# Kernel optimization log

Hardware: AMD Instinct MI355X
Metric: run time of the kernel (lower is better)

## Reference

```python
import jax, jax.numpy as jnp
import numpy as np

W_WIN = 21  # window size (init arg w)
N_HEADS = 8
HEAD_DIM = 64

def setup_inputs() -> dict:
    key = jax.random.key(0)
    ks = jax.random.split(key, 6)
    b, c, l, d = 8, 2, 2048, 512
    x = jax.random.normal(ks[0], (b, c, l, d), dtype=jnp.float32)
    Wqkv = jax.random.normal(ks[1], (d, 3 * d), dtype=jnp.float32) * (1.0 / np.sqrt(d))
    bqkv = jax.random.normal(ks[2], (3 * d,), dtype=jnp.float32) * 0.02
    bias_rw = jax.random.uniform(ks[3], (N_HEADS, HEAD_DIM), dtype=jnp.float32,
                                 minval=-1.0 / np.sqrt(HEAD_DIM), maxval=1.0 / np.sqrt(HEAD_DIM))
    Wout = jax.random.normal(ks[4], (d, d), dtype=jnp.float32) * (1.0 / np.sqrt(d))
    bout = jax.random.normal(ks[5], (d,), dtype=jnp.float32) * 0.02
    return {"x": x, "Wqkv": Wqkv, "bqkv": bqkv, "bias_rw": bias_rw, "Wout": Wout, "bout": bout}

def reference(x, Wqkv, bqkv, bias_rw, Wout, bout):
    b, c, l, d = x.shape
    H, hd = bias_rw.shape
    B = b * c
    w_half = W_WIN // 2

    xf = x.reshape(B, l, d)
    qkv = xf @ Wqkv + bqkv                      # [B, l, 3d]
    q, k, v = jnp.split(qkv, 3, axis=-1)
    q = q.reshape(B, l, H, hd) * (hd ** -0.5)
    k = k.reshape(B, l, H, hd)
    v = v.reshape(B, l, H, hd)

    qk = q + bias_rw                            # bias_r_w added to queries (q_r branch is dead code)

    # banded scores: offset o corresponds to key position p + (o - w_half)
    kp = jnp.pad(k, ((0, 0), (w_half, w_half), (0, 0), (0, 0)))
    vp = jnp.pad(v, ((0, 0), (w_half, w_half), (0, 0), (0, 0)))
    scores = jnp.stack(
        [jnp.einsum('blnh,blnh->bln', qk, jax.lax.dynamic_slice_in_dim(kp, o, l, axis=1))
         for o in range(W_WIN)], axis=-1)       # [B, l, H, w]

    pos = jnp.arange(l)[:, None] + (jnp.arange(W_WIN)[None, :] - w_half)  # [l, w]
    valid = (pos >= 0) & (pos < l)
    neg = -jnp.finfo(scores.dtype).max
    scores = jnp.where(valid[None, :, None, :], scores, neg)

    A = jax.nn.softmax(scores, axis=-1)         # [B, l, H, w]; dropout(0.2) is identity at eval

    z = jnp.zeros_like(v)
    for o in range(W_WIN):
        z = z + A[:, :, :, o, None] * jax.lax.dynamic_slice_in_dim(vp, o, l, axis=1)

    z = z.reshape(b, c, l, H * hd)
    return z @ Wout + bout
```

## Files before the change

### kernel.cpp

```cpp
#include <hip/hip_runtime.h>
#include <stdint.h>

typedef __bf16 bf16x8 __attribute__((ext_vector_type(8)));
typedef float f32x4 __attribute__((ext_vector_type(4)));
typedef unsigned short u16x8 __attribute__((ext_vector_type(8)));

__device__ __forceinline__ unsigned short f2bf(float f) {
  uint32_t u = __builtin_bit_cast(uint32_t, f);
  u += 0x7FFFu + ((u >> 16) & 1u);
  return (unsigned short)(u >> 16);
}
__device__ __forceinline__ float bf2f(unsigned short h) {
  uint32_t u = ((uint32_t)h) << 16;
  return __builtin_bit_cast(float, u);
}

__device__ __forceinline__ void gload_lds16(const void* g, void* l) {
  __builtin_amdgcn_global_load_lds(
      (const __attribute__((address_space(1))) uint32_t*)g,
      (__attribute__((address_space(3))) uint32_t*)l,
      16, 0, 0);
}


__global__ __launch_bounds__(256) void k_cvt_x(const float* __restrict__ x,
                                               unsigned short* __restrict__ xb, int n4) {
  int stride = gridDim.x * blockDim.x;
  for (int i = blockIdx.x * blockDim.x + threadIdx.x; i < n4; i += stride) {
    float4 v = reinterpret_cast<const float4*>(x)[i];
    ushort4 o;
    o.x = f2bf(v.x); o.y = f2bf(v.y); o.z = f2bf(v.z); o.w = f2bf(v.w);
    reinterpret_cast<ushort4*>(xb)[i] = o;
  }
}

__global__ __launch_bounds__(256) void k_cvt_wT(const float* __restrict__ w,
                                                unsigned short* __restrict__ wt, int K, int N) {
  int total = K * N;
  int stride = gridDim.x * blockDim.x;
  for (int i = blockIdx.x * blockDim.x + threadIdx.x; i < total; i += stride) {
    int n = i / K;
    int k = i - n * K;
    wt[i] = f2bf(w[(size_t)k * N + n]);
  }
}

template <int EPI>
__global__ __launch_bounds__(512, 4) void k_gemm256x128(
    const unsigned short* __restrict__ A,
    const unsigned short* __restrict__ Bt,
    const float* __restrict__ bias,
    const float* __restrict__ brw,
    unsigned short* __restrict__ oq,
    unsigned short* __restrict__ okk,
    unsigned short* __restrict__ ov,
    float* __restrict__ of,
    int Ntiles) {
  __shared__ __align__(128) char lds[73728];

  int cpx = gridDim.x >> 3;
  int bid = (blockIdx.x & 7) * cpx + (blockIdx.x >> 3);
  int bm = bid / Ntiles;
  int bn = bid - bm * Ntiles;
  int row0 = bm << 8;
  int col0 = bn << 7;
  int t = threadIdx.x;
  int lane = t & 63;
  int w = t >> 6;
  int wm = w >> 1;
  int wn = w & 1;
  int lr = lane & 15;
  int lk = lane >> 4;

  const unsigned short* Ab = A + (size_t)row0 * 512;
  const unsigned short* Bb = Bt + (size_t)col0 * 512;

  f32x4 acc[4][4];
#pragma unroll
  for (int i = 0; i < 4; ++i)
#pragma unroll
    for (int j = 0; j < 4; ++j) acc[i][j] = f32x4{0.f, 0.f, 0.f, 0.f};

  auto stage = [&](int kt, int b) {
    int k0 = kt << 5;
    char* base = lds + b * 24576;
#pragma unroll
    for (int i = 0; i < 2; ++i) {
      int o = (i << 9) + t;
      int row = o >> 2;
      int slot = o & 3;
      int gk = k0 + ((slot ^ ((row >> 1) & 3)) << 3);
      gload_lds16(Ab + (size_t)row * 512 + gk, base + (o << 4));
    }
    {
      int o = t;
      int row = o >> 2;
      int slot = o & 3;
      int gk = k0 + ((slot ^ ((row >> 1) & 3)) << 3);
      gload_lds16(Bb + (size_t)row * 512 + gk, base + 16384 + (o << 4));
    }
  };

  auto tile = [&](int b, int ktpf, int bpf, bool pf) {
    const char* Abuf = lds + b * 24576;
    const char* Bbuf = Abuf + 16384;
    bf16x8 af[4], bfs[4];
#pragma unroll
    for (int nf = 0; nf < 4; ++nf) {
      int r = (wn << 6) + (nf << 4) + lr;
      bfs[nf] = *reinterpret_cast<const bf16x8*>(Bbuf + (r << 6) + ((lk ^ ((r >> 1) & 3)) << 4));
    }
#pragma unroll
    for (int mf = 0; mf < 4; ++mf) {
      int r = (wm << 6) + (mf << 4) + lr;
      af[mf] = *reinterpret_cast<const bf16x8*>(Abuf + (r << 6) + ((lk ^ ((r >> 1) & 3)) << 4));
    }
    if (pf) stage(ktpf, bpf);
    __builtin_amdgcn_s_setprio(1);
#pragma unroll
    for (int mf = 0; mf < 4; ++mf)
#pragma unroll
      for (int nf = 0; nf < 4; ++nf)
        acc[mf][nf] = __builtin_amdgcn_mfma_f32_16x16x32_bf16(af[mf], bfs[nf], acc[mf][nf], 0, 0, 0);
    __builtin_amdgcn_s_setprio(0);
  };

  stage(0, 0);
  stage(1, 1);
  asm volatile("s_waitcnt vmcnt(3)" ::: "memory");
  __builtin_amdgcn_s_barrier();

  int cb = 0;
#pragma unroll 1
  for (int kt = 0; kt < 14; ++kt) {
    int pb = cb + 2; if (pb >= 3) pb -= 3;
    tile(cb, kt + 2, pb, true);
    asm volatile("s_waitcnt vmcnt(3)" ::: "memory");
    __builtin_amdgcn_s_barrier();
    ++cb; if (cb >= 3) cb -= 3;
  }
  tile(cb, 0, 0, false);
  asm volatile("s_waitcnt vmcnt(0)" ::: "memory");
  __builtin_amdgcn_s_barrier();
  ++cb; if (cb >= 3) cb -= 3;
  tile(cb, 0, 0, false);
  __builtin_amdgcn_s_barrier();

  if (EPI == 0) {
    char* ep = lds + (w << 13);
    int gc0 = col0 + (wn << 6);
    int part = gc0 >> 9;
    int hh = (gc0 & 511) >> 6;
    unsigned short* dst = (part == 0) ? oq : (part == 1) ? okk : ov;
    float bvv[4], rbv[4];
#pragma unroll
    for (int nf = 0; nf < 4; ++nf) {
      int cc = (nf << 4) + lr;
      bvv[nf] = bias[gc0 + cc];
      rbv[nf] = (part == 0) ? brw[(gc0 & 511) + cc] : 0.f;
    }
#pragma unroll
    for (int mf = 0; mf < 4; ++mf) {
#pragma unroll
      for (int nf = 0; nf < 4; ++nf) {
        int cc = (nf << 4) + lr;
#pragma unroll
        for (int j = 0; j < 4; ++j) {
          int r = (mf << 4) + (lk << 2) + j;
          float v = acc[mf][nf][j] + bvv[nf];
          if (part == 0) v = v * 0.125f + rbv[nf];
          int byte = (r << 7) + ((((cc >> 3) ^ (r & 7))) << 4) + ((cc & 7) << 1);
          *reinterpret_cast<unsigned short*>(ep + byte) = f2bf(v);
        }
      }
    }
    asm volatile("s_waitcnt lgkmcnt(0)" ::: "memory");
    __builtin_amdgcn_sched_barrier(0);
    int b0 = row0 >> 11;
    size_t base = (size_t)(b0 * 8 + hh) * 2048;
#pragma unroll
    for (int i = 0; i < 8; ++i) {
      int rr = (i << 3) + (lane >> 3);
      int ch = lane & 7;
      int byte = (rr << 7) + ((ch ^ (rr & 7)) << 4);
      u16x8 val = *reinterpret_cast<const u16x8*>(ep + byte);
      int gl = (row0 + (wm << 6) + rr) & 2047;
      *reinterpret_cast<u16x8*>(dst + ((base + gl) << 6) + (ch << 3)) = val;
    }
  } else {
#pragma unroll
    for (int mf = 0; mf < 4; ++mf) {
#pragma unroll
      for (int j = 0; j < 4; ++j) {
        int gr = row0 + (wm << 6) + (mf << 4) + (lk << 2) + j;
#pragma unroll
        for (int nf = 0; nf < 4; ++nf) {
          int gc = col0 + (wn << 6) + (nf << 4) + lr;
          of[(size_t)gr * 512 + gc] = acc[mf][nf][j] + bias[gc];
        }
      }
    }
  }
}

__global__ __launch_bounds__(256) void k_attn_mfma(
    const unsigned short* __restrict__ qb,
    const unsigned short* __restrict__ kb,
    const unsigned short* __restrict__ vb,
    unsigned short* __restrict__ zb) {
  __shared__ __align__(128) unsigned short smem[13312];

  int t = threadIdx.x;
  int bh = blockIdx.x >> 5;
  int l0 = (blockIdx.x & 31) << 6;
  size_t slab = (size_t)bh << 17;

#pragma unroll
  for (int i = 0; i < 3; ++i) {
    int kloc = (i << 5) + (t >> 3);
    int c8 = (t & 7) << 3;
    int kg = l0 - 10 + kloc;
    kg = kg < 0 ? 0 : (kg > 2047 ? 2047 : kg);
    u16x8 v = *reinterpret_cast<const u16x8*>(vb + slab + ((size_t)kg << 6) + c8);
#pragma unroll
    for (int e = 0; e < 8; ++e) smem[(c8 + e) * 104 + kloc] = v[e];
  }

  int lane = t & 63;
  int w = t >> 6;
  int lr = lane & 15;
  int lk = lane >> 4;

  const unsigned short* qp = qb + slab + ((size_t)(l0 + (w << 4) + lr) << 6) + (lk << 3);
  bf16x8 qf0 = *reinterpret_cast<const bf16x8*>(qp);
  bf16x8 qf1 = *reinterpret_cast<const bf16x8*>(qp + 32);

  f32x4 sacc[6];
#pragma unroll
  for (int kt = 0; kt < 6; ++kt) {
    int kl = (kt << 4) + lr;
    int kg = l0 - 10 + kl;
    int kgc = kg < 0 ? 0 : (kg > 2047 ? 2047 : kg);
    const unsigned short* kp = kb + slab + ((size_t)kgc << 6) + (lk << 3);
    bf16x8 kf0 = *reinterpret_cast<const bf16x8*>(kp);
    bf16x8 kf1 = *reinterpret_cast<const bf16x8*>(kp + 32);
    f32x4 z4 = {0.f, 0.f, 0.f, 0.f};
    z4 = __builtin_amdgcn_mfma_f32_16x16x32_bf16(qf0, kf0, z4, 0, 0, 0);
    sacc[kt] = __builtin_amdgcn_mfma_f32_16x16x32_bf16(qf1, kf1, z4, 0, 0, 0);
  }

  int qlb = (w << 4) + (lk << 2);
  float p[6][4];
  float minv[4];
#pragma unroll
  for (int j = 0; j < 4; ++j) {
    int ql = qlb + j;
    float mx = -1e30f;
#pragma unroll
    for (int kt = 0; kt < 6; ++kt) {
      int kl = (kt << 4) + lr;
      int kg = l0 - 10 + kl;
      bool valid = (kl >= ql) && (kl <= ql + 20) && (kg >= 0) && (kg < 2048);
      float sv = valid ? sacc[kt][j] : -1e30f;
      p[kt][j] = sv;
      mx = fmaxf(mx, sv);
    }
    mx = fmaxf(mx, __shfl_xor(mx, 1));
    mx = fmaxf(mx, __shfl_xor(mx, 2));
    mx = fmaxf(mx, __shfl_xor(mx, 4));
    mx = fmaxf(mx, __shfl_xor(mx, 8));
    float sum = 0.f;
#pragma unroll
    for (int kt = 0; kt < 6; ++kt) {
      float e = (p[kt][j] > -1e29f) ? __expf(p[kt][j] - mx) : 0.f;
      p[kt][j] = e;
      sum += e;
    }
    sum += __shfl_xor(sum, 1);
    sum += __shfl_xor(sum, 2);
    sum += __shfl_xor(sum, 4);
    sum += __shfl_xor(sum, 8);
    minv[j] = 1.f / sum;
  }

  unsigned short* P = smem + 6656;
#pragma unroll
  for (int j = 0; j < 4; ++j)
#pragma unroll
    for (int kt = 0; kt < 6; ++kt)
      P[(qlb + j) * 104 + (kt << 4) + lr] = f2bf(p[kt][j]);

  __syncthreads();

  f32x4 zacc[4];
#pragma unroll
  for (int dt = 0; dt < 4; ++dt) zacc[dt] = f32x4{0.f, 0.f, 0.f, 0.f};
  bf16x8 pf[3];
#pragma unroll
  for (int s3 = 0; s3 < 3; ++s3)
    pf[s3] = *reinterpret_cast<const bf16x8*>(P + ((w << 4) + lr) * 104 + (s3 << 5) + (lk << 3));
#pragma unroll
  for (int dt = 0; dt < 4; ++dt) {
#pragma unroll
    for (int s3 = 0; s3 < 3; ++s3) {
      bf16x8 vf = *reinterpret_cast<const bf16x8*>(smem + ((dt << 4) + lr) * 104 + (s3 << 5) + (lk << 3));
      zacc[dt] = __builtin_amdgcn_mfma_f32_16x16x32_bf16(pf[s3], vf, zacc[dt], 0, 0, 0);
    }
  }

  __syncthreads();

  unsigned short* ZL = smem;
#pragma unroll
  for (int dt = 0; dt < 4; ++dt)
#pragma unroll
    for (int j = 0; j < 4; ++j)
      ZL[(qlb + j) * 80 + (dt << 4) + lr] = f2bf(zacc[dt][j] * minv[j]);
  asm volatile("s_waitcnt lgkmcnt(0)" ::: "memory");
  __builtin_amdgcn_sched_barrier(0);

  int b = bh >> 3, h = bh & 7;
#pragma unroll
  for (int i = 0; i < 2; ++i) {
    int rr = (w << 4) + (i << 3) + (lane >> 3);
    int ch = (lane & 7) << 3;
    u16x8 val = *reinterpret_cast<const u16x8*>(ZL + rr * 80 + ch);
    size_t orow = (size_t)(b * 2048 + l0 + rr);
    *reinterpret_cast<u16x8*>(zb + (orow << 9) + (h << 6) + ch) = val;
  }
}


extern "C" void kernel_launch(void* const* d_in, const int* in_sizes, int n_in,
                              void* d_out, int out_size, void* d_ws, size_t ws_size,
                              hipStream_t stream) {
  (void)in_sizes; (void)n_in; (void)out_size; (void)ws_size;
  const float* x    = (const float*)d_in[0];
  const float* Wqkv = (const float*)d_in[1];
  const float* bqkv = (const float*)d_in[2];
  const float* brw  = (const float*)d_in[3];
  const float* Wout = (const float*)d_in[4];
  const float* bout = (const float*)d_in[5];
  float* out = (float*)d_out;

  char* ws = (char*)d_ws;
  unsigned short* xb  = (unsigned short*)(ws);
  unsigned short* wqT = (unsigned short*)(ws + 33554432);
  unsigned short* woT = (unsigned short*)(ws + 35127296);
  unsigned short* qs  = (unsigned short*)(ws + 35651584);
  unsigned short* kbf = (unsigned short*)(ws + 69206016);
  unsigned short* vbf = (unsigned short*)(ws + 102760448);
  unsigned short* zb  = xb;

  k_cvt_x<<<2048, 256, 0, stream>>>(x, xb, 16777216 / 4);
  k_cvt_wT<<<768, 256, 0, stream>>>(Wqkv, wqT, 512, 1536);
  k_cvt_wT<<<256, 256, 0, stream>>>(Wout, woT, 512, 512);
  k_gemm256x128<0><<<1536, 512, 0, stream>>>(xb, wqT, bqkv, brw, qs, kbf, vbf, nullptr, 12);
  k_attn_mfma<<<4096, 256, 0, stream>>>(qs, kbf, vbf, zb);
  k_gemm256x128<1><<<512, 512, 0, stream>>>(zb, woT, bout, nullptr, nullptr, nullptr, nullptr, out, 4);
}
```

Before: 151.2 us.

## Fuse fp32-to-bf16 conversion of x into QKV GEMM and merge weight casts

Removes the standalone x conversion kernel: the QKV GEMM now streams fp32 x tiles straight into LDS and converts to bf16 while building MFMA fragments. The two weight-transpose kernels are merged into one launch. This drops the 32MB bf16 write and re-read of x, but the GEMM now reads twice the A bytes per tile and falls back from a 3-stage to a 2-stage LDS pipeline with a full vmcnt(0) wait each iteration, which may expose more memory latency.

```diff
diff --git a/kernel.cpp b/kernel.cpp
--- a/kernel.cpp
+++ b/kernel.cpp
@@ -22,41 +22,37 @@
       16, 0, 0);
 }
 
-
-__global__ __launch_bounds__(256) void k_cvt_x(const float* __restrict__ x,
-                                               unsigned short* __restrict__ xb, int n4) {
-  int stride = gridDim.x * blockDim.x;
-  for (int i = blockIdx.x * blockDim.x + threadIdx.x; i < n4; i += stride) {
-    float4 v = reinterpret_cast<const float4*>(x)[i];
-    ushort4 o;
-    o.x = f2bf(v.x); o.y = f2bf(v.y); o.z = f2bf(v.z); o.w = f2bf(v.w);
-    reinterpret_cast<ushort4*>(xb)[i] = o;
-  }
-}
-
-__global__ __launch_bounds__(256) void k_cvt_wT(const float* __restrict__ w,
-                                                unsigned short* __restrict__ wt, int K, int N) {
-  int total = K * N;
-  int stride = gridDim.x * blockDim.x;
-  for (int i = blockIdx.x * blockDim.x + threadIdx.x; i < total; i += stride) {
-    int n = i / K;
-    int k = i - n * K;
-    wt[i] = f2bf(w[(size_t)k * N + n]);
-  }
-}
-
-template <int EPI>
-__global__ __launch_bounds__(512, 4) void k_gemm256x128(
-    const unsigned short* __restrict__ A,
+__global__ __launch_bounds__(256) void k_cvt_w(
+    const float* __restrict__ Wqkv, const float* __restrict__ Wout,
+    unsigned short* __restrict__ wqT, unsigned short* __restrict__ woT) {
+  int b = blockIdx.x;
+  if (b < 768) {
+    int stride = 768 * 256;
+    for (int i = b * 256 + threadIdx.x; i < 786432; i += stride) {
+      int n = i >> 9;
+      int k = i & 511;
+      wqT[i] = f2bf(Wqkv[(size_t)k * 1536 + n]);
+    }
+  } else {
+    int stride = 256 * 256;
+    for (int i = (b - 768) * 256 + threadIdx.x; i < 262144; i += stride) {
+      int n = i >> 9;
+      int k = i & 511;
+      woT[i] = f2bf(Wout[(size_t)k * 512 + n]);
+    }
+  }
+}
+
+__global__ __launch_bounds__(512, 4) void k_g1f(
+    const float* __restrict__ X,
     const unsigned short* __restrict__ Bt,
     const float* __restrict__ bias,
     const float* __restrict__ brw,
     unsigned short* __restrict__ oq,
     unsigned short* __restrict__ okk,
     unsigned short* __restrict__ ov,
-    float* __restrict__ of,
     int Ntiles) {
-  __shared__ __align__(128) char lds[73728];
+  __shared__ __align__(128) char lds[81920];
 
   int cpx = gridDim.x >> 3;
   int bid = (blockIdx.x & 7) * cpx + (blockIdx.x >> 3);
@@ -72,6 +68,145 @@
   int lr = lane & 15;
   int lk = lane >> 4;
 
+  const float* Xb = X + (size_t)row0 * 512;
+  const unsigned short* Bb = Bt + (size_t)col0 * 512;
+
+  f32x4 acc[4][4];
+#pragma unroll
+  for (int i = 0; i < 4; ++i)
+#pragma unroll
+    for (int j = 0; j < 4; ++j) acc[i][j] = f32x4{0.f, 0.f, 0.f, 0.f};
+
+  auto stage = [&](int kt) {
+    char* base = lds + ((kt & 1) ? 40960 : 0);
+    int k0 = kt << 5;
+#pragma unroll
+    for (int i = 0; i < 4; ++i) {
+      int o = (i << 9) + t;
+      int row = o >> 3;
+      int s = o & 7;
+      gload_lds16(Xb + (size_t)row * 512 + k0 + ((s ^ (row & 7)) << 2),
+                  base + (o << 4));
+    }
+    {
+      int o = t;
+      int row = o >> 2;
+      int s = o & 3;
+      gload_lds16(Bb + (size_t)row * 512 + (kt << 5) + ((s ^ ((row >> 1) & 3)) << 3),
+                  base + 32768 + (o << 4));
+    }
+  };
+
+  auto tile = [&](int kt) {
+    const char* base = lds + ((kt & 1) ? 40960 : 0);
+    const char* Bbuf = base + 32768;
+    bf16x8 af[4], bfs[4];
+#pragma unroll
+    for (int nf = 0; nf < 4; ++nf) {
+      int r = (wn << 6) + (nf << 4) + lr;
+      bfs[nf] = *reinterpret_cast<const bf16x8*>(Bbuf + (r << 6) + ((lk ^ ((r >> 1) & 3)) << 4));
+    }
+#pragma unroll
+    for (int mf = 0; mf < 4; ++mf) {
+      int r = (wm << 6) + (mf << 4) + lr;
+      int c0 = (lk << 1);
+      f32x4 lo = *reinterpret_cast<const f32x4*>(base + (r << 7) + ((c0 ^ (r & 7)) << 4));
+      f32x4 hi = *reinterpret_cast<const f32x4*>(base + (r << 7) + (((c0 + 1) ^ (r & 7)) << 4));
+      bf16x8 a;
+#pragma unroll
+      for (int e = 0; e < 4; ++e) {
+        a[e] = (__bf16)lo[e];
+        a[4 + e] = (__bf16)hi[e];
+      }
+      af[mf] = a;
+    }
+    __builtin_amdgcn_s_setprio(1);
+#pragma unroll
+    for (int mf = 0; mf < 4; ++mf)
+#pragma unroll
+      for (int nf = 0; nf < 4; ++nf)
+        acc[mf][nf] = __builtin_amdgcn_mfma_f32_16x16x32_bf16(af[mf], bfs[nf], acc[mf][nf], 0, 0, 0);
+    __builtin_amdgcn_s_setprio(0);
+  };
+
+  stage(0);
+  asm volatile("s_waitcnt vmcnt(0)" ::: "memory");
+  __builtin_amdgcn_s_barrier();
+
+#pragma unroll 1
+  for (int kt = 0; kt < 15; ++kt) {
+    stage(kt + 1);
+    tile(kt);
+    asm volatile("s_waitcnt vmcnt(0)" ::: "memory");
+    __builtin_amdgcn_s_barrier();
+  }
+  tile(15);
+  __builtin_amdgcn_s_barrier();
+
+  char* ep = lds + (w << 13);
+  int gc0 = col0 + (wn << 6);
+  int part = gc0 >> 9;
+  int hh = (gc0 & 511) >> 6;
+  unsigned short* dst = (part == 0) ? oq : (part == 1) ? okk : ov;
+  float bvv[4], rbv[4];
+#pragma unroll
+  for (int nf = 0; nf < 4; ++nf) {
+    int cc = (nf << 4) + lr;
+    bvv[nf] = bias[gc0 + cc];
+    rbv[nf] = (part == 0) ? brw[(gc0 & 511) + cc] : 0.f;
+  }
+#pragma unroll
+  for (int mf = 0; mf < 4; ++mf) {
+#pragma unroll
+    for (int nf = 0; nf < 4; ++nf) {
+      int cc = (nf << 4) + lr;
+#pragma unroll
+      for (int j = 0; j < 4; ++j) {
+        int r = (mf << 4) + (lk << 2) + j;
+        float v = acc[mf][nf][j] + bvv[nf];
+        if (part == 0) v = v * 0.125f + rbv[nf];
+        int byte = (r << 7) + ((((cc >> 3) ^ (r & 7))) << 4) + ((cc & 7) << 1);
+        *reinterpret_cast<unsigned short*>(ep + byte) = f2bf(v);
+      }
+    }
+  }
+  asm volatile("s_waitcnt lgkmcnt(0)" ::: "memory");
+  __builtin_amdgcn_sched_barrier(0);
+  int b0 = row0 >> 11;
+  size_t base = (size_t)(b0 * 8 + hh) * 2048;
+#pragma unroll
+  for (int i = 0; i < 8; ++i) {
+    int rr = (i << 3) + (lane >> 3);
+    int ch = lane & 7;
+    int byte = (rr << 7) + ((ch ^ (rr & 7)) << 4);
+    u16x8 val = *reinterpret_cast<const u16x8*>(ep + byte);
+    int gl = (row0 + (wm << 6) + rr) & 2047;
+    *reinterpret_cast<u16x8*>(dst + ((base + gl) << 6) + (ch << 3)) = val;
+  }
+}
+
+__global__ __launch_bounds__(512, 4) void k_gemm2(
+    const unsigned short* __restrict__ A,
+    const unsigned short* __restrict__ Bt,
+    const float* __restrict__ bias,
+    float* __restrict__ of,
+    int Ntiles) {
+  __shared__ __align__(128) char lds[73728];
+
+  int cpx = gridDim.x >> 3;
+  int bid = (blockIdx.x & 7) * cpx + (blockIdx.x >> 3);
+  int bm = bid / Ntiles;
+  int bn = bid - bm * Ntiles;
+  int row0 = bm << 8;
+  int col0 = bn << 7;
+  int t = threadIdx.x;
+  int lane = t & 63;
+  int w = t >> 6;
+  int wm = w >> 1;
+  int wn = w & 1;
+  int lr = lane & 15;
+  int lk = lane >> 4;
+
   const unsigned short* Ab = A + (size_t)row0 * 512;
   const unsigned short* Bb = Bt + (size_t)col0 * 512;
 
@@ -144,60 +279,16 @@
   __builtin_amdgcn_s_barrier();
   ++cb; if (cb >= 3) cb -= 3;
   tile(cb, 0, 0, false);
-  __builtin_amdgcn_s_barrier();
-
-  if (EPI == 0) {
-    char* ep = lds + (w << 13);
-    int gc0 = col0 + (wn << 6);
-    int part = gc0 >> 9;
-    int hh = (gc0 & 511) >> 6;
-    unsigned short* dst = (part == 0) ? oq : (part == 1) ? okk : ov;
-    float bvv[4], rbv[4];
-#pragma unroll
-    for (int nf = 0; nf < 4; ++nf) {
-      int cc = (nf << 4) + lr;
-      bvv[nf] = bias[gc0 + cc];
-      rbv[nf] = (part == 0) ? brw[(gc0 & 511) + cc] : 0.f;
-    }
-#pragma unroll
-    for (int mf = 0; mf < 4; ++mf) {
+
+#pragma unroll
+  for (int mf = 0; mf < 4; ++mf) {
+#pragma unroll
+    for (int j = 0; j < 4; ++j) {
+      int gr = row0 + (wm << 6) + (mf << 4) + (lk << 2) + j;
 #pragma unroll
       for (int nf = 0; nf < 4; ++nf) {
-        int cc = (nf << 4) + lr;
-#pragma unroll
-        for (int j = 0; j < 4; ++j) {
-          int r = (mf << 4) + (lk << 2) + j;
-          float v = acc[mf][nf][j] + bvv[nf];
-          if (part == 0) v = v * 0.125f + rbv[nf];
-          int byte = (r << 7) + ((((cc >> 3) ^ (r & 7))) << 4) + ((cc & 7) << 1);
-          *reinterpret_cast<unsigned short*>(ep + byte) = f2bf(v);
-        }
-      }
-    }
-    asm volatile("s_waitcnt lgkmcnt(0)" ::: "memory");
-    __builtin_amdgcn_sched_barrier(0);
-    int b0 = row0 >> 11;
-    size_t base = (size_t)(b0 * 8 + hh) * 2048;
-#pragma unroll
-    for (int i = 0; i < 8; ++i) {
-      int rr = (i << 3) + (lane >> 3);
-      int ch = lane & 7;
-      int byte = (rr << 7) + ((ch ^ (rr & 7)) << 4);
-      u16x8 val = *reinterpret_cast<const u16x8*>(ep + byte);
-      int gl = (row0 + (wm << 6) + rr) & 2047;
-      *reinterpret_cast<u16x8*>(dst + ((base + gl) << 6) + (ch << 3)) = val;
-    }
-  } else {
-#pragma unroll
-    for (int mf = 0; mf < 4; ++mf) {
-#pragma unroll
-      for (int j = 0; j < 4; ++j) {
-        int gr = row0 + (wm << 6) + (mf << 4) + (lk << 2) + j;
-#pragma unroll
-        for (int nf = 0; nf < 4; ++nf) {
-          int gc = col0 + (wn << 6) + (nf << 4) + lr;
-          of[(size_t)gr * 512 + gc] = acc[mf][nf][j] + bias[gc];
-        }
+        int gc = col0 + (wn << 6) + (nf << 4) + lr;
+        of[(size_t)gr * 512 + gc] = acc[mf][nf][j] + bias[gc];
       }
     }
   }
@@ -344,18 +435,15 @@
   float* out = (float*)d_out;
 
   char* ws = (char*)d_ws;
-  unsigned short* xb  = (unsigned short*)(ws);
+  unsigned short* zb  = (unsigned short*)(ws);
   unsigned short* wqT = (unsigned short*)(ws + 33554432);
   unsigned short* woT = (unsigned short*)(ws + 35127296);
   unsigned short* qs  = (unsigned short*)(ws + 35651584);
   unsigned short* kbf = (unsigned short*)(ws + 69206016);
   unsigned short* vbf = (unsigned short*)(ws + 102760448);
-  unsigned short* zb  = xb;
-
-  k_cvt_x<<<2048, 256, 0, stream>>>(x, xb, 16777216 / 4);
-  k_cvt_wT<<<768, 256, 0, stream>>>(Wqkv, wqT, 512, 1536);
-  k_cvt_wT<<<256, 256, 0, stream>>>(Wout, woT, 512, 512);
-  k_gemm256x128<0><<<1536, 512, 0, stream>>>(xb, wqT, bqkv, brw, qs, kbf, vbf, nullptr, 12);
+
+  k_cvt_w<<<1024, 256, 0, stream>>>(Wqkv, Wout, wqT, woT);
+  k_g1f<<<1536, 512, 0, stream>>>(x, wqT, bqkv, brw, qs, kbf, vbf, 12);
   k_attn_mfma<<<4096, 256, 0, stream>>>(qs, kbf, vbf, zb);
-  k_gemm256x128<1><<<512, 512, 0, stream>>>(zb, woT, bout, nullptr, nullptr, nullptr, nullptr, out, 4);
-}
+  k_gemm2<<<512, 512, 0, stream>>>(zb, woT, bout, out, 4);
+}
```

After: 164.6 us. 8.9% more time.
